# Kernel optimization log

Hardware: AMD Instinct MI355X
Metric: run time of the kernel (lower is better)

## Reference

```python
import jax, jax.numpy as jnp
import numpy as np

B, S, D, H, DH = 8192, 64, 32, 4, 8

def setup_inputs() -> dict:
    key = jax.random.key(0)
    ks = jax.random.split(key, 10)
    lim = 1.0 / np.sqrt(D)
    def lin(k):
        kw, kb = jax.random.split(k)
        W = jax.random.uniform(kw, (D, D), jnp.float32, -lim, lim)
        b = jax.random.uniform(kb, (D,), jnp.float32, -lim, lim)
        return W, b
    Wq, bq = lin(ks[0]); Wk, bk = lin(ks[1]); Wv, bv = lin(ks[2]); Wp, bp = lin(ks[3])
    x = jax.random.normal(ks[4], (B, S, D), jnp.float32)
    always_attend_upto = jax.random.randint(ks[5], (B,), 0, 64, jnp.int64 if jax.config.jax_enable_x64 else jnp.int32)
    return {"x": x, "always_attend_upto": always_attend_upto,
            "Wq": Wq, "bq": bq, "Wk": Wk, "bk": bk, "Wv": Wv, "bv": bv, "Wp": Wp, "bp": bp}

def reference(x, always_attend_upto, Wq, bq, Wk, bk, Wv, bv, Wp, bp):
    # QKV projections (torch Linear: y = x @ W.T + b)
    def heads(W, b):
        y = x @ W.T + b                      # [B,S,D]
        return y.reshape(B, S, H, DH).transpose(0, 2, 1, 3)  # [B,H,S,DH]
    q, k, v = heads(Wq, bq), heads(Wk, bk), heads(Wv, bv)
    score = jnp.einsum('bhqd,bhkd->bhqk', q, k) / jnp.sqrt(jnp.float32(DH))
    # prefix-LM mask: allowed if causal (j<=i) OR key in prefix (j < length[b])
    i = jnp.arange(S)[:, None]
    j = jnp.arange(S)[None, :]
    causal = j <= i                                        # [S,S]
    prefix = j[None, :, :] < always_attend_upto[:, None, None]  # [B,S,S]
    allowed = (causal[None] | prefix)[:, None, :, :]       # [B,1,S,S]
    score = jnp.where(allowed, score, -jnp.inf)
    attn = jax.nn.softmax(score, axis=-1)
    out = jnp.einsum('bhqk,bhkd->bhqd', attn, v)           # [B,H,S,DH]
    out = out.transpose(0, 2, 1, 3).reshape(B, S, D)
    return out @ Wp.T + bp
```

## Files before the change

### kernel.cpp

```cpp
#include <hip/hip_runtime.h>
#include <cstdint>
#include <cstddef>

#define NB 8192

typedef __attribute__((ext_vector_type(8))) short short8;
typedef __attribute__((ext_vector_type(4))) float f32x4;

union S8U { short8 s; unsigned u[4]; uint4 v; };
union FI { float f; int i; unsigned u; };

static __device__ __forceinline__ unsigned pk2(float a, float b) {
    unsigned short ua = __builtin_bit_cast(unsigned short, (__bf16)a);
    unsigned short ub = __builtin_bit_cast(unsigned short, (__bf16)b);
    return (unsigned)ua | ((unsigned)ub << 16);
}

#define MFMA __builtin_amdgcn_mfma_f32_16x16x32_bf16
#define BPERM __builtin_amdgcn_ds_bpermute

__global__ __launch_bounds__(128, 4) void fused_attn_mfma(
    const float* __restrict__ x,
    const int*   __restrict__ aatt,
    const float* __restrict__ Wq, const float* __restrict__ bq,
    const float* __restrict__ Wk, const float* __restrict__ bk,
    const float* __restrict__ Wv, const float* __restrict__ bv,
    const float* __restrict__ Wp, const float* __restrict__ bp,
    float* __restrict__ out)
{
    __shared__ __align__(16) short klds[64][40];
    __shared__ __align__(16) short vbt[33][72];
    __shared__ __align__(16) short psl[2][2][16][40];

    const int tid  = threadIdx.x;
    const int w    = tid >> 6;
    const int lane = tid & 63;
    const int q4   = lane >> 4;
    const int l15  = lane & 15;
    const int b    = blockIdx.x;

    const int aab = aatt[b];
    const unsigned bmask = (q4 == 0) ? 0xFFFFFFFFu : 0u;

    int cmpv[4];
#pragma unroll
    for (int it = 0; it < 4; ++it) cmpv[it] = max(l15 + 16*it, aab - 1) - q4*4;

    short8 xa[4];
    const float* xb = x + (size_t)b * 64 * 32;
#pragma unroll
    for (int nt = 0; nt < 4; ++nt) {
        const float* p = xb + (nt*16 + l15)*32 + q4*8;
        float4 u0 = *(const float4*)p;
        float4 u1 = *(const float4*)(p + 4);
        S8U t;
        t.u[0] = pk2(u0.x, u0.y); t.u[1] = pk2(u0.z, u0.w);
        t.u[2] = pk2(u1.x, u1.y); t.u[3] = pk2(u1.z, u1.w);
        xa[nt] = t.s;
    }

    auto wrow = [&](const float* W, int row) -> short8 {
        const float* p = W + row*32 + q4*8;
        float4 u0 = *(const float4*)p;
        float4 u1 = *(const float4*)(p + 4);
        S8U t;
        t.u[0] = pk2(u0.x, u0.y); t.u[1] = pk2(u0.z, u0.w);
        t.u[2] = pk2(u1.x, u1.y); t.u[3] = pk2(u1.z, u1.w);
        return t.s;
    };

    const float escale = 0.35355339059327373f * 1.4426950408889634f;

    unsigned qpk01[4], qpk23[4];
    {
        short8 wa = wrow(Wq, 16*w + l15);
        float4 b4 = *(const float4*)(bq + 16*w + q4*4);
#pragma unroll
        for (int nt = 0; nt < 4; ++nt) {
            f32x4 acc = {0.f,0.f,0.f,0.f};
            acc = MFMA(wa, xa[nt], acc, 0,0,0);
            qpk01[nt] = pk2((acc[0]+b4.x)*escale, (acc[1]+b4.y)*escale);
            qpk23[nt] = pk2((acc[2]+b4.z)*escale, (acc[3]+b4.w)*escale);
        }
    }
    {
        short8 wa = wrow(Wk, 16*w + l15);
        float4 b4 = *(const float4*)(bk + 16*w + q4*4);
#pragma unroll
        for (int nt = 0; nt < 4; ++nt) {
            f32x4 acc = {0.f,0.f,0.f,0.f};
            acc = MFMA(wa, xa[nt], acc, 0,0,0);
            uint2 w2;
            w2.x = pk2(acc[0]+b4.x, acc[1]+b4.y);
            w2.y = pk2(acc[2]+b4.z, acc[3]+b4.w);
            *(uint2*)&klds[nt*16 + l15][16*w + q4*4] = w2;
        }
    }
    {
        short8 wv = wrow(Wv, 16*w + l15);
        const float bvv = bv[16*w + l15];
#pragma unroll
        for (int mt = 0; mt < 4; ++mt) {
            f32x4 acc = {0.f,0.f,0.f,0.f};
            acc = MFMA(xa[mt], wv, acc, 0,0,0);
            uint2 w2;
            w2.x = pk2(acc[0]+bvv, acc[1]+bvv);
            w2.y = pk2(acc[2]+bvv, acc[3]+bvv);
            *(uint2*)&vbt[16*w + l15][mt*16 + q4*4] = w2;
        }
    }
    if (q4 == 0) {
        uint2 ones; ones.x = 0x3F803F80u; ones.y = 0x3F803F80u;
        *(uint2*)&vbt[32][l15*4] = ones;
    }

#pragma unroll
    for (int hl = 0; hl < 2; ++hl) {
        const int idxA = (32*hl + l15) * 4;
        const int idxB = idxA + 64;

        short8 sqb[4];
#pragma unroll
        for (int it = 0; it < 4; ++it) {
            S8U t;
            t.u[0] = (unsigned)BPERM(idxA, (int)qpk01[it]) & bmask;
            t.u[1] = (unsigned)BPERM(idxA, (int)qpk23[it]) & bmask;
            t.u[2] = (unsigned)BPERM(idxB, (int)qpk01[it]) & bmask;
            t.u[3] = (unsigned)BPERM(idxB, (int)qpk23[it]) & bmask;
            sqb[it] = t.s;
        }

        const int avrow = (l15 < 8) ? (16*w + 8*hl + l15) : 32;
        S8U av[2];
        av[0].v = *(const uint4*)&vbt[avrow][q4*8];
        av[1].v = *(const uint4*)&vbt[avrow][32 + q4*8];

        f32x4 oacch[4];
#pragma unroll
        for (int it = 0; it < 4; ++it) oacch[it] = (f32x4){0.f,0.f,0.f,0.f};

#pragma unroll
        for (int tk = 0; tk < 8; ++tk) {
            const int jb = tk >> 2, it = tk & 3;
#pragma unroll
            for (int jt = 0; jt < 2; ++jt) {
                S8U kt; kt.v = *(const uint4*)&klds[jb*32 + jt*16 + l15][16*w + 8*hl];
                f32x4 sacc = {0.f,0.f,0.f,0.f};
                sacc = MFMA(kt.s, sqb[it], sacc, 0,0,0);
                float e[4];
#pragma unroll
                for (int r = 0; r < 4; ++r) {
                    float ee = __builtin_amdgcn_exp2f(sacc[r]);
                    e[r] = (jb*32 + jt*16 + r <= cmpv[it]) ? ee : 0.0f;
                }
                uint2 pw; pw.x = pk2(e[0], e[1]); pw.y = pk2(e[2], e[3]);
                *(uint2*)&psl[w][tk & 1][l15][jt*16 + q4*4] = pw;
            }
            if (tk > 0) {
                const int pj = (tk - 1) >> 2, pi = (tk - 1) & 3;
                S8U pb; pb.v = *(const uint4*)&psl[w][(tk - 1) & 1][l15][q4*8];
                oacch[pi] = MFMA(av[pj].s, pb.s, oacch[pi], 0,0,0);
            }
        }
        {
            S8U pb; pb.v = *(const uint4*)&psl[w][1][l15][q4*8];
            oacch[3] = MFMA(av[1].s, pb.s, oacch[3], 0,0,0);
        }

#pragma unroll
        for (int it = 0; it < 4; ++it) {
            FI s; s.i = BPERM((32 + l15) * 4, __builtin_bit_cast(int, oacch[it][0]));
            const float inv = __builtin_amdgcn_rcpf(s.f);
            const unsigned o01 = pk2(oacch[it][0]*inv, oacch[it][1]*inv);
            const unsigned o23 = pk2(oacch[it][2]*inv, oacch[it][3]*inv);
            if (q4 < 2) {
                uint2 ow; ow.x = o01; ow.y = o23;
                *(uint2*)&klds[it*16 + l15][(2*w + hl)*8 + q4*4] = ow;
            }
        }
    }

    __syncthreads();

    short8 wpb[2];
#pragma unroll
    for (int nt = 0; nt < 2; ++nt) wpb[nt] = wrow(Wp, nt*16 + l15);

    const float bpv[2] = { bp[l15], bp[16 + l15] };
    float* ob = out + (size_t)b * 64 * 32;
#pragma unroll
    for (int u = 0; u < 2; ++u) {
        S8U oa; oa.v = *(const uint4*)&klds[(2*w + u)*16 + l15][q4*8];
#pragma unroll
        for (int nt = 0; nt < 2; ++nt) {
            f32x4 y = {0.f,0.f,0.f,0.f};
            y = MFMA(oa.s, wpb[nt], y, 0,0,0);
#pragma unroll
            for (int r = 0; r < 4; ++r)
                ob[((2*w + u)*16 + q4*4 + r)*32 + nt*16 + l15] = y[r] + bpv[nt];
        }
    }
}

extern "C" void kernel_launch(void* const* d_in, const int* in_sizes, int n_in,
                              void* d_out, int out_size, void* d_ws, size_t ws_size,
                              hipStream_t stream) {
    const float* x  = (const float*)d_in[0];
    const int*   aa = (const int*)d_in[1];
    const float* Wq = (const float*)d_in[2];
    const float* bq = (const float*)d_in[3];
    const float* Wk = (const float*)d_in[4];
    const float* bk = (const float*)d_in[5];
    const float* Wv = (const float*)d_in[6];
    const float* bv = (const float*)d_in[7];
    const float* Wp = (const float*)d_in[8];
    const float* bp = (const float*)d_in[9];
    float* out = (float*)d_out;

    dim3 grid(NB), block(128);
    hipLaunchKernelGGL(fused_attn_mfma, grid, block, 0, stream,
                       x, aa, Wq, bq, Wk, bk, Wv, bv, Wp, bp, out);
}
```

Baseline: 51.06 us.

## Keep softmax probabilities in registers by permuting V and K layouts for MFMA

Removes the per-warp LDS staging buffer for exponentiated scores. The score MFMA output fragments are packed directly into the B operand of the PV MFMA. To make that valid, the V^T tile is stored in LDS with a permuted key ordering, and K is read with a matching layout. Extra zero padding is written into the K buffer's unused columns. This cuts LDS round-trips and the software pipelining across iterations, at the cost of relying on a permuted reduction order being mathematically equivalent.

```diff
diff --git a/kernel.cpp b/kernel.cpp
--- a/kernel.cpp
+++ b/kernel.cpp
@@ -30,7 +30,6 @@
 {
     __shared__ __align__(16) short klds[64][40];
     __shared__ __align__(16) short vbt[33][72];
-    __shared__ __align__(16) short psl[2][2][16][40];
 
     const int tid  = threadIdx.x;
     const int w    = tid >> 6;
@@ -96,6 +95,10 @@
             *(uint2*)&klds[nt*16 + l15][16*w + q4*4] = w2;
         }
     }
+    if (w == 1) {
+        uint4 z4; z4.x = 0u; z4.y = 0u; z4.z = 0u; z4.w = 0u;
+        *(uint4*)&klds[lane][32] = z4;
+    }
     {
         short8 wv = wrow(Wv, 16*w + l15);
         const float bvv = bv[16*w + l15];
@@ -106,7 +109,7 @@
             uint2 w2;
             w2.x = pk2(acc[0]+bvv, acc[1]+bvv);
             w2.y = pk2(acc[2]+bvv, acc[3]+bvv);
-            *(uint2*)&vbt[16*w + l15][mt*16 + q4*4] = w2;
+            *(uint2*)&vbt[16*w + l15][(mt >> 1)*32 + q4*8 + (mt & 1)*4] = w2;
         }
     }
     if (q4 == 0) {
@@ -131,40 +134,45 @@
         }
 
         const int avrow = (l15 < 8) ? (16*w + 8*hl + l15) : 32;
-        S8U av[2];
-        av[0].v = *(const uint4*)&vbt[avrow][q4*8];
-        av[1].v = *(const uint4*)&vbt[avrow][32 + q4*8];
 
         f32x4 oacch[4];
 #pragma unroll
         for (int it = 0; it < 4; ++it) oacch[it] = (f32x4){0.f,0.f,0.f,0.f};
 
 #pragma unroll
-        for (int tk = 0; tk < 8; ++tk) {
-            const int jb = tk >> 2, it = tk & 3;
-#pragma unroll
-            for (int jt = 0; jt < 2; ++jt) {
-                S8U kt; kt.v = *(const uint4*)&klds[jb*32 + jt*16 + l15][16*w + 8*hl];
-                f32x4 sacc = {0.f,0.f,0.f,0.f};
-                sacc = MFMA(kt.s, sqb[it], sacc, 0,0,0);
-                float e[4];
-#pragma unroll
-                for (int r = 0; r < 4; ++r) {
-                    float ee = __builtin_amdgcn_exp2f(sacc[r]);
-                    e[r] = (jb*32 + jt*16 + r <= cmpv[it]) ? ee : 0.0f;
+        for (int jb = 0; jb < 2; ++jb) {
+            S8U ska0, ska1, av;
+            ska0.v = *(const uint4*)&klds[jb*32 + l15][16*w + 8*hl];
+            ska1.v = *(const uint4*)&klds[jb*32 + 16 + l15][16*w + 8*hl];
+            av.v   = *(const uint4*)&vbt[avrow][jb*32 + q4*8];
+
+#pragma unroll
+            for (int it = 0; it < 4; ++it) {
+                S8U pb;
+                {
+                    f32x4 sacc = {0.f,0.f,0.f,0.f};
+                    sacc = MFMA(ska0.s, sqb[it], sacc, 0,0,0);
+                    float e[4];
+#pragma unroll
+                    for (int r = 0; r < 4; ++r) {
+                        float ee = __builtin_amdgcn_exp2f(sacc[r]);
+                        e[r] = (jb*32 + r <= cmpv[it]) ? ee : 0.0f;
+                    }
+                    pb.u[0] = pk2(e[0], e[1]); pb.u[1] = pk2(e[2], e[3]);
                 }
-                uint2 pw; pw.x = pk2(e[0], e[1]); pw.y = pk2(e[2], e[3]);
-                *(uint2*)&psl[w][tk & 1][l15][jt*16 + q4*4] = pw;
+                {
+                    f32x4 sacc = {0.f,0.f,0.f,0.f};
+                    sacc = MFMA(ska1.s, sqb[it], sacc, 0,0,0);
+                    float e[4];
+#pragma unroll
+                    for (int r = 0; r < 4; ++r) {
+                        float ee = __builtin_amdgcn_exp2f(sacc[r]);
+                        e[r] = (jb*32 + 16 + r <= cmpv[it]) ? ee : 0.0f;
+                    }
+                    pb.u[2] = pk2(e[0], e[1]); pb.u[3] = pk2(e[2], e[3]);
+                }
+                oacch[it] = MFMA(av.s, pb.s, oacch[it], 0,0,0);
             }
-            if (tk > 0) {
-                const int pj = (tk - 1) >> 2, pi = (tk - 1) & 3;
-                S8U pb; pb.v = *(const uint4*)&psl[w][(tk - 1) & 1][l15][q4*8];
-                oacch[pi] = MFMA(av[pj].s, pb.s, oacch[pi], 0,0,0);
-            }
-        }
-        {
-            S8U pb; pb.v = *(const uint4*)&psl[w][1][l15][q4*8];
-            oacch[3] = MFMA(av[1].s, pb.s, oacch[3], 0,0,0);
         }
 
 #pragma unroll
```

Measured after the change: 51.51 us. No clear change (+0.9%).
